# Kernel tuning notes

Measured on AMD Instinct MI355X. Metric: run time of the kernel, lower is better.

The kernel has to match this reference:

```python
import jax, jax.numpy as jnp
import numpy as np

B, T, U, V, C, K = 64, 800, 64, 60, 512, 10

def setup_inputs() -> dict:
    key = jax.random.key(0)
    ks = jax.random.split(key, 8)
    x = jax.random.normal(ks[0], (B, T, 3), dtype=jnp.float32)
    char_ids = jax.random.randint(ks[1], (B, U), 0, V)
    onehots = jax.nn.one_hot(char_ids, V, dtype=jnp.float32)  # [B,U,V]
    text_lens = jax.random.randint(ks[2], (B, 1), 32, U + 1).astype(jnp.float32)
    w_old = jnp.zeros((B, V), jnp.float32)
    kappa_old = jnp.zeros((B, K), jnp.float32)
    prev_h = jnp.zeros((B, C), jnp.float32)
    prev_c = jnp.zeros((B, C), jnp.float32)
    s = 0.08
    W_ih = jax.random.normal(ks[3], (4 * C, 3 + V), jnp.float32) * s
    W_hh = jax.random.normal(ks[4], (4 * C, C), jnp.float32) * s
    b_ih = jnp.zeros((4 * C,), jnp.float32)
    b_hh = jnp.zeros((4 * C,), jnp.float32)
    win_W = jax.random.normal(ks[5], (3 * K, C), jnp.float32) * s
    win_b = jnp.zeros((3 * K,), jnp.float32)
    return dict(x=x, onehots=onehots, text_lens=text_lens, w_old=w_old,
                kappa_old=kappa_old, prev_h=prev_h, prev_c=prev_c,
                W_ih=W_ih, W_hh=W_hh, b_ih=b_ih, b_hh=b_hh,
                win_W=win_W, win_b=win_b)

def reference(x, onehots, text_lens, w_old, kappa_old, prev_h, prev_c,
              W_ih, W_hh, b_ih, b_hh, win_W, win_b):
    Upad = onehots.shape[1]
    idx = jnp.arange(Upad + 1, dtype=x.dtype)          # text-position indices
    scale = Upad / text_lens                           # [B,1] length normalization

    def step(carry, xt):
        h, c, w, kap = carry
        inp = jnp.concatenate([xt, w], axis=-1)        # [B, 3+V]
        gates = inp @ W_ih.T + b_ih + h @ W_hh.T + b_hh
        i, f, g, o = jnp.split(gates, 4, axis=-1)
        i = jax.nn.sigmoid(i); f = jax.nn.sigmoid(f)
        g = jnp.tanh(g);      o = jax.nn.sigmoid(o)
        c = f * c + i * g
        h = o * jnp.tanh(c)
        # Gaussian-mixture attention window
        p = jnp.exp(h @ win_W.T + win_b)               # [B, 3K]
        alpha, beta, dkap = jnp.split(p, 3, axis=-1)   # each [B, K]
        kap = kap + dkap
        gravity = -beta[:, :, None] * (kap[:, :, None] - idx) ** 2   # [B,K,U+1]
        phi = jnp.sum(alpha[:, :, None] * jnp.exp(gravity), axis=1) * scale  # [B,U+1]
        w = jnp.einsum('bu,buv->bv', phi[:, :Upad], onehots)
        return (h, c, w, kap), (h, w, phi)

    xs = jnp.swapaxes(x, 0, 1)                         # [T,B,3]
    (h, c, w, kap), (hs, ws, phis) = jax.lax.scan(
        step, (prev_h, prev_c, w_old, kappa_old), xs)
    ws = jnp.swapaxes(ws, 0, 1)                        # [B,T,V]
    hs = jnp.swapaxes(hs, 0, 1)                        # [B,T,C]
    return ws, hs, h, c, w, kap, phis[-1]
```

## Files before the change

kernel.cpp:

```cpp
#include <hip/hip_runtime.h>
#include <math.h>

#define B_  64
#define T_  800
#define U_  64
#define V_  60
#define C_  512
#define K_  10
#define KXF 584
#define NWG 256
#define NTH 512
#define KQ  8
#define KSL 72
#define NB  4
#define GRPWG 16

typedef unsigned long long ull;
typedef _Float16 f16;
typedef _Float16 f16x2 __attribute__((ext_vector_type(2)));

#define HL_N (2*B_*C_)

__device__ __forceinline__ float sigm(float v)  { return 1.f/(1.f+__expf(-v)); }
__device__ __forceinline__ float tanhx(float v) { return 1.f - 2.f/(__expf(2.f*v)+1.f); }

__device__ __forceinline__ float dot2(f16x2 a, f16x2 b, float c) {
  return __builtin_amdgcn_fdot2(a, b, c, false);
}
__device__ __forceinline__ f16x2 bc2(unsigned u) {
  return __builtin_bit_cast(f16x2, u);
}
__device__ __forceinline__ float wfetch(const float* __restrict__ W_ih,
                                        const float* __restrict__ W_hh,
                                        int row, int k) {
  if (k < 3)  return W_ih[row*63 + k];
  if (k == 3) return 0.f;
  if (k < 64) return W_ih[row*63 + (k-1)];
  return W_hh[row*C_ + (k-64)];
}

__device__ __forceinline__ void ld4x16_loc(const ull* p0, const ull* p1,
                                           const ull* p2, const ull* p3,
                                           ulonglong2& r0, ulonglong2& r1,
                                           ulonglong2& r2, ulonglong2& r3) {
  asm volatile(
    "global_load_dwordx4 %0, %4, off sc0\n\t"
    "global_load_dwordx4 %1, %5, off sc0\n\t"
    "global_load_dwordx4 %2, %6, off sc0\n\t"
    "global_load_dwordx4 %3, %7, off sc0\n\t"
    "s_waitcnt vmcnt(0)"
    : "=&v"(r0), "=&v"(r1), "=&v"(r2), "=&v"(r3)
    : "v"(p0), "v"(p1), "v"(p2), "v"(p3) : "memory");
}
__device__ __forceinline__ void ld4x16_mal(const ull* p0, const ull* p1,
                                           const ull* p2, const ull* p3,
                                           ulonglong2& r0, ulonglong2& r1,
                                           ulonglong2& r2, ulonglong2& r3) {
  asm volatile(
    "global_load_dwordx4 %0, %4, off sc0 sc1\n\t"
    "global_load_dwordx4 %1, %5, off sc0 sc1\n\t"
    "global_load_dwordx4 %2, %6, off sc0 sc1\n\t"
    "global_load_dwordx4 %3, %7, off sc0 sc1\n\t"
    "s_waitcnt vmcnt(0)"
    : "=&v"(r0), "=&v"(r1), "=&v"(r2), "=&v"(r3)
    : "v"(p0), "v"(p1), "v"(p2), "v"(p3) : "memory");
}

__global__ __launch_bounds__(NTH, 2)
void lstm_attn_persistent(
    const float* __restrict__ x,
    const float* __restrict__ onehots,
    const float* __restrict__ text_lens,
    const float* __restrict__ w_old,
    const float* __restrict__ kappa_old,
    const float* __restrict__ prev_h,
    const float* __restrict__ prev_c,
    const float* __restrict__ W_ih,
    const float* __restrict__ W_hh,
    const float* __restrict__ b_ih,
    const float* __restrict__ b_hh,
    const float* __restrict__ win_W,
    const float* __restrict__ win_b,
    ull* __restrict__ hl,
    float* __restrict__ out)
{
  __builtin_amdgcn_fence(__ATOMIC_ACQUIRE, "agent");

  const long OUT_WS  = 0;
  const long OUT_HS  = (long)B_*T_*V_;
  const long OUT_H   = OUT_HS + (long)B_*T_*C_;
  const long OUT_C   = OUT_H  + (long)B_*C_;
  const long OUT_W   = OUT_C  + (long)B_*C_;
  const long OUT_KAP = OUT_W  + (long)B_*V_;
  const long OUT_PHI = OUT_KAP+ (long)B_*K_;

  ull* hg = hl + HL_N;

  const int tid  = threadIdx.x;
  const int kq   = tid >> 6;
  const int lane = tid & 63;
  const int bid  = blockIdx.x;
  const int grp  = bid & 15;
  const int gblk = bid >> 4;
  const int b0   = grp * NB;

  const int rlo = kq ? (kq*KSL - 64) : 0;
  const int rhi = kq*64 + 64;

  __shared__ __align__(16) f16   hxh[NB][KXF];
  __shared__ __align__(16) float wbuf[NB][64];
  __shared__ __align__(16) float part[KQ][NB][2][68];
  __shared__ __align__(16) float wpart[KQ][NB][68];
  __shared__ float p_lds[NB][32];
  __shared__ float kap_lds[NB][12];
  __shared__ float scale_lds[NB];
  __shared__ float winb_lds[32];
  __shared__ int   ids_lds[NB][64];

  f16x2 Wh[2][KSL/2];
  float bias2[2];
  #pragma unroll
  for (int s = 0; s < 2; ++s) {
    int gp   = gblk*128 + lane + 64*s;
    int gate = gp & 3;
    int ch   = gp >> 2;
    int row  = gate*C_ + ch;
    #pragma unroll
    for (int i = 0; i < KSL/2; ++i) {
      float w0 = wfetch(W_ih, W_hh, row, kq*KSL + 2*i);
      float w1 = wfetch(W_ih, W_hh, row, kq*KSL + 2*i + 1);
      f16x2 p; p[0] = (f16)w0; p[1] = (f16)w1;
      Wh[s][i] = p;
    }
    bias2[s] = b_ih[row] + b_hh[row];
  }

  const int wj = lane % 30;
  const int wh = (lane < 60) ? (lane / 30) : 0;
  f16x2 winh[16];
  #pragma unroll
  for (int i = 0; i < 16; ++i) {
    f16x2 p;
    p[0] = (f16)win_W[wj*C_ + kq*64 + wh*32 + 2*i];
    p[1] = (f16)win_W[wj*C_ + kq*64 + wh*32 + 2*i + 1];
    winh[i] = p;
  }

  const int ub    = tid >> 5;
  const int chloc = tid & 31;
  const int mych  = gblk*32 + chloc;
  float c_reg = 0.f;
  if (tid < 128) c_reg = prev_c[(long)(b0 + ub)*C_ + mych];

  for (int i = tid; i < NB*576; i += NTH) {
    int bb = i / 576, k = i % 576;
    int b = b0 + bb;
    float v;
    if      (k < 3)  v = x[((long)b*T_ + 0)*3 + k];
    else if (k < 4)  v = 0.f;
    else if (k < 64) v = w_old[b*V_ + (k-4)];
    else             v = prev_h[(long)b*C_ + (k-64)];
    hxh[bb][k] = (f16)v;
  }
  for (int i = tid; i < NB*64; i += NTH) {
    int bb = i >> 6, j = i & 63;
    wbuf[bb][j] = (j < 60) ? w_old[(b0+bb)*V_ + j] : 0.f;
  }
  for (int i = tid; i < NB*K_; i += NTH)
    kap_lds[i/K_][i%K_] = kappa_old[(b0 + i/K_)*K_ + i%K_];
  if (tid < NB) scale_lds[tid] = (float)U_ / text_lens[b0 + tid];
  if (tid < 30) winb_lds[tid] = win_b[tid];
  for (int i = tid; i < NB*U_; i += NTH) {
    int bb = i / U_, u = i % U_;
    const float* oh = onehots + ((long)(b0+bb)*U_ + u)*V_;
    int best = 0; float bv = oh[0];
    for (int vv = 1; vv < V_; ++vv) { float q = oh[vv]; if (q > bv) { bv = q; best = vv; } }
    ids_lds[bb][u] = best;
  }
  __syncthreads();

  bool use_mall = false;

  for (int t = 0; t < T_; ++t) {
    float acc[NB][2];
    #pragma unroll
    for (int bb = 0; bb < NB; ++bb) {
      acc[bb][0] = (kq == 0) ? bias2[0] : 0.f;
      acc[bb][1] = (kq == 0) ? bias2[1] : 0.f;
    }
    #pragma unroll
    for (int bb = 0; bb < NB; ++bb) {
      const uint4* hb = (const uint4*)&hxh[bb][kq*KSL];
      float a0 = acc[bb][0], a1 = acc[bb][1];
      #pragma unroll
      for (int j = 0; j < 9; ++j) {
        uint4 hv = hb[j];
        f16x2 h0 = bc2(hv.x), h1 = bc2(hv.y), h2 = bc2(hv.z), h3 = bc2(hv.w);
        a0 = dot2(Wh[0][4*j+0], h0, a0);  a1 = dot2(Wh[1][4*j+0], h0, a1);
        a0 = dot2(Wh[0][4*j+1], h1, a0);  a1 = dot2(Wh[1][4*j+1], h1, a1);
        a0 = dot2(Wh[0][4*j+2], h2, a0);  a1 = dot2(Wh[1][4*j+2], h2, a1);
        a0 = dot2(Wh[0][4*j+3], h3, a0);  a1 = dot2(Wh[1][4*j+3], h3, a1);
      }
      acc[bb][0] = a0; acc[bb][1] = a1;
    }
    #pragma unroll
    for (int bb = 0; bb < NB; ++bb) {
      part[kq][bb][0][lane] = acc[bb][0];
      part[kq][bb][1][lane] = acc[bb][1];
    }
    __syncthreads();

    if (tid < 128) {
      const int sr = chloc >> 4, c4 = (chloc & 15) * 4;
      float4 s = make_float4(0.f, 0.f, 0.f, 0.f);
      #pragma unroll
      for (int q = 0; q < KQ; ++q) {
        float4 v = *(const float4*)&part[q][ub][sr][c4];
        s.x += v.x; s.y += v.y; s.z += v.z; s.w += v.w;
      }
      float ig = sigm(s.x), fg = sigm(s.y), gg = tanhx(s.z), og = sigm(s.w);
      float c = fg*c_reg + ig*gg;
      c_reg = c;
      float h = og * tanhx(c);
      int b = b0 + ub;
      ull pk = ((ull)(unsigned)(t+1) << 32) | (ull)__float_as_uint(h);
      long hidx = (long)(t&1)*B_*C_ + (long)b*C_ + mych;
      hl[hidx] = pk;
      __hip_atomic_store(&hg[hidx], pk,
                         __ATOMIC_RELAXED, __HIP_MEMORY_SCOPE_AGENT);
      out[OUT_HS + ((long)b*T_ + t)*C_ + mych] = h;
      if (t == T_-1) {
        out[OUT_H + (long)b*C_ + mych] = h;
        out[OUT_C + (long)b*C_ + mych] = c;
      }
    }

    {
      const int want = t + 1;
      const int ch = rlo + lane*2;
      const bool act = ch < rhi;
      const long boff = (long)(t&1)*B_*C_ + ch;
      ulonglong2 r0, r1, r2, r3;
      r0.x=r0.y=r1.x=r1.y=r2.x=r2.y=r3.x=r3.y=0;
      int tries = 0;
      while (true) {
        bool ok = true;
        if (act) {
          const ull* base = use_mall ? hg : hl;
          const ull* p0 = base + boff + (long)(b0+0)*C_;
          const ull* p1 = base + boff + (long)(b0+1)*C_;
          const ull* p2 = base + boff + (long)(b0+2)*C_;
          const ull* p3 = base + boff + (long)(b0+3)*C_;
          if (use_mall) ld4x16_mal(p0,p1,p2,p3, r0,r1,r2,r3);
          else          ld4x16_loc(p0,p1,p2,p3, r0,r1,r2,r3);
          ok = (int)(r0.x>>32) >= want && (int)(r0.y>>32) >= want &&
               (int)(r1.x>>32) >= want && (int)(r1.y>>32) >= want &&
               (int)(r2.x>>32) >= want && (int)(r2.y>>32) >= want &&
               (int)(r3.x>>32) >= want && (int)(r3.y>>32) >= want;
        }
        if (__all(ok)) break;
        if (!use_mall && ++tries > 200) use_mall = true;
      }
      if (act) {
        f16x2 p;
        p[0] = (f16)__uint_as_float((unsigned)r0.x);
        p[1] = (f16)__uint_as_float((unsigned)r0.y);
        *(unsigned*)&hxh[0][64+ch] = __builtin_bit_cast(unsigned, p);
        p[0] = (f16)__uint_as_float((unsigned)r1.x);
        p[1] = (f16)__uint_as_float((unsigned)r1.y);
        *(unsigned*)&hxh[1][64+ch] = __builtin_bit_cast(unsigned, p);
        p[0] = (f16)__uint_as_float((unsigned)r2.x);
        p[1] = (f16)__uint_as_float((unsigned)r2.y);
        *(unsigned*)&hxh[2][64+ch] = __builtin_bit_cast(unsigned, p);
        p[0] = (f16)__uint_as_float((unsigned)r3.x);
        p[1] = (f16)__uint_as_float((unsigned)r3.y);
        *(unsigned*)&hxh[3][64+ch] = __builtin_bit_cast(unsigned, p);
      }
    }

    #pragma unroll
    for (int bb = 0; bb < NB; ++bb) {
      const uint4* hb = (const uint4*)&hxh[bb][64 + kq*64 + wh*32];
      float a = 0.f;
      #pragma unroll
      for (int j = 0; j < 4; ++j) {
        uint4 hv = hb[j];
        a = dot2(winh[4*j+0], bc2(hv.x), a);
        a = dot2(winh[4*j+1], bc2(hv.y), a);
        a = dot2(winh[4*j+2], bc2(hv.z), a);
        a = dot2(winh[4*j+3], bc2(hv.w), a);
      }
      if (lane < 60) wpart[kq][bb][lane] = a;
    }
    __syncthreads();

    if (kq < NB) {
      const int bb = kq;
      if (lane < 30) {
        float s = 0.f;
        #pragma unroll
        for (int q = 0; q < KQ; ++q) s += wpart[q][bb][lane] + wpart[q][bb][30+lane];
        float p = __expf(s + winb_lds[lane]);
        p_lds[bb][lane] = p;
        if (lane >= 20) {
          float nk = kap_lds[bb][lane-20] + p;
          kap_lds[bb][lane-20] = nk;
          if (t == T_-1 && gblk == 0) out[OUT_KAP + (b0+bb)*K_ + (lane-20)] = nk;
        }
      }
      if (lane < 60) wbuf[bb][lane] = 0.f;
      else if (lane < 63) {
        int tn = t + 1;
        hxh[bb][lane-60] = (f16)((tn < T_) ? x[((long)(b0+bb)*T_ + tn)*3 + (lane-60)] : 0.f);
      }
      {
        float s = 0.f;
        float uf = (float)lane;
        #pragma unroll
        for (int k = 0; k < K_; ++k) {
          float d = kap_lds[bb][k] - uf;
          s += p_lds[bb][k] * __expf(-p_lds[bb][10+k]*d*d);
        }
        float phiv = s * scale_lds[bb];
        atomicAdd(&wbuf[bb][ids_lds[bb][lane]], phiv);
        if (t == T_-1 && gblk == 0) {
          out[OUT_PHI + (b0+bb)*65 + lane] = phiv;
          if (lane == 0) {
            float s2 = 0.f;
            #pragma unroll
            for (int k = 0; k < K_; ++k) {
              float d = kap_lds[bb][k] - 64.f;
              s2 += p_lds[bb][k] * __expf(-p_lds[bb][10+k]*d*d);
            }
            out[OUT_PHI + (b0+bb)*65 + 64] = s2 * scale_lds[bb];
          }
        }
      }
      if (lane < 60) {
        float wv = wbuf[bb][lane];
        hxh[bb][4+lane] = (f16)wv;
        if (gblk == (t & 15)) {
          out[OUT_WS + ((long)(b0+bb)*T_ + t)*V_ + lane] = wv;
          if (t == T_-1) out[OUT_W + (b0+bb)*V_ + lane] = wv;
        }
      }
    }
    __syncthreads();
  }
}

extern "C" void kernel_launch(void* const* d_in, const int* in_sizes, int n_in,
                              void* d_out, int out_size, void* d_ws, size_t ws_size,
                              hipStream_t stream) {
  const float* x         = (const float*)d_in[0];
  const float* onehots   = (const float*)d_in[1];
  const float* text_lens = (const float*)d_in[2];
  const float* w_old     = (const float*)d_in[3];
  const float* kappa_old = (const float*)d_in[4];
  const float* prev_h    = (const float*)d_in[5];
  const float* prev_c    = (const float*)d_in[6];
  const float* W_ih      = (const float*)d_in[7];
  const float* W_hh      = (const float*)d_in[8];
  const float* b_ih      = (const float*)d_in[9];
  const float* b_hh      = (const float*)d_in[10];
  const float* win_W     = (const float*)d_in[11];
  const float* win_b     = (const float*)d_in[12];
  ull*   hl  = (ull*)d_ws;
  float* out = (float*)d_out;

  hipMemsetAsync(d_ws, 0, 2ull*HL_N*sizeof(ull), stream);

  lstm_attn_persistent<<<NWG, NTH, 0, stream>>>(
      x, onehots, text_lens, w_old, kappa_old, prev_h, prev_c,
      W_ih, W_hh, b_ih, b_hh, win_W, win_b, hl, out);
}
```

Before: 4.116 ms.

## Assign workgroups to batch groups by XCD via atomic counters

Each workgroup reads its hardware XCD id and claims a slot in a batch group tied to that XCD through atomic counters, instead of deriving the group from blockIdx. The aim is to keep all 16 workgroups that exchange h state for a batch group on the same XCD, so the per-step exchange stays in that XCD's L2. Each workgroup then checks whether its group members really share one XCD, and if they do not it sets use_mall to take the cross-XCD path. This adds startup atomics and a spin-wait, and it relies on the memset now also zeroing the counters.

```diff
diff --git a/kernel.cpp b/kernel.cpp
--- a/kernel.cpp
+++ b/kernel.cpp
@@ -94,18 +94,13 @@
   const long OUT_KAP = OUT_W  + (long)B_*V_;
   const long OUT_PHI = OUT_KAP+ (long)B_*K_;
 
-  ull* hg = hl + HL_N;
+  ull* hg   = hl + HL_N;
+  int* gcnt = (int*)(hl + 2*HL_N);
+  int* xtab = gcnt + 16;
 
   const int tid  = threadIdx.x;
   const int kq   = tid >> 6;
   const int lane = tid & 63;
-  const int bid  = blockIdx.x;
-  const int grp  = bid & 15;
-  const int gblk = bid >> 4;
-  const int b0   = grp * NB;
-
-  const int rlo = kq ? (kq*KSL - 64) : 0;
-  const int rhi = kq*64 + 64;
 
   __shared__ __align__(16) f16   hxh[NB][KXF];
   __shared__ __align__(16) float wbuf[NB][64];
@@ -116,6 +111,50 @@
   __shared__ float scale_lds[NB];
   __shared__ float winb_lds[32];
   __shared__ int   ids_lds[NB][64];
+  __shared__ int   meta[2];
+  __shared__ int   cons[16];
+
+  if (tid == 0) {
+    unsigned xcd = __builtin_amdgcn_s_getreg(63508) & 7;
+    int g = -1, s = -1;
+    #pragma unroll 1
+    for (int probe = 0; probe < 2 && g < 0; ++probe) {
+      int gg = (int)xcd*2 + probe;
+      int ss = atomicAdd(&gcnt[gg], 1);
+      if (ss < GRPWG) { g = gg; s = ss; }
+    }
+    #pragma unroll 1
+    for (int gg = 0; gg < 16 && g < 0; ++gg) {
+      int ss = atomicAdd(&gcnt[gg], 1);
+      if (ss < GRPWG) { g = gg; s = ss; }
+    }
+    meta[0] = g; meta[1] = s;
+    __hip_atomic_store(&xtab[g*GRPWG + s], (int)xcd + 1,
+                       __ATOMIC_RELAXED, __HIP_MEMORY_SCOPE_AGENT);
+  }
+  __syncthreads();
+  const int grp  = meta[0];
+  const int gblk = meta[1];
+  const int b0   = grp * NB;
+  if (tid < GRPWG) {
+    int v;
+    do {
+      v = __hip_atomic_load(&xtab[grp*GRPWG + tid],
+                            __ATOMIC_RELAXED, __HIP_MEMORY_SCOPE_AGENT);
+    } while (v == 0);
+    cons[tid] = v;
+  }
+  __syncthreads();
+  bool use_mall;
+  {
+    int x0 = cons[0], same = 1;
+    #pragma unroll
+    for (int i = 1; i < GRPWG; ++i) same &= (cons[i] == x0);
+    use_mall = !same;
+  }
+
+  const int rlo = kq ? (kq*KSL - 64) : 0;
+  const int rhi = kq*64 + 64;
 
   f16x2 Wh[2][KSL/2];
   float bias2[2];
@@ -178,8 +217,6 @@
     ids_lds[bb][u] = best;
   }
   __syncthreads();
-
-  bool use_mall = false;
 
   for (int t = 0; t < T_; ++t) {
     float acc[NB][2];
@@ -368,7 +405,7 @@
   ull*   hl  = (ull*)d_ws;
   float* out = (float*)d_out;
 
-  hipMemsetAsync(d_ws, 0, 2ull*HL_N*sizeof(ull), stream);
+  hipMemsetAsync(d_ws, 0, 2ull*HL_N*sizeof(ull) + 4096, stream);
 
   lstm_attn_persistent<<<NWG, NTH, 0, stream>>>(
       x, onehots, text_lens, w_old, kappa_old, prev_h, prev_c,
```

Result: no change. 4.092 ms (-0.6%).
